# Kernel optimization log

Measured on AMD Instinct MI355X. Metric: run time of the kernel, lower is better.

## Reference

```python
import jax, jax.numpy as jnp
import numpy as np

EPS = 1e-12
N_NODES = 100000
N_EDGES = 1600000
IN_CH = 8
N_CLASSES = 16
MAX_ORDER = 1
N_RINGS = 2


def setup_inputs() -> dict:
    key = jax.random.key(0)
    k0, k1, k2, k3, k4 = jax.random.split(key, 5)
    x = jax.random.normal(k0, (N_NODES, IN_CH), dtype=jnp.float32)
    edge_index = jax.random.randint(k1, (2, N_EDGES), 0, N_NODES)
    precomp = jax.random.normal(k2, (N_EDGES, MAX_ORDER + 1, N_RINGS, 2), dtype=jnp.float32)
    connection = jax.random.normal(k3, (N_EDGES, 2), dtype=jnp.float32)
    # n_orders = (prev_order+1)*(max_order+1) with default prev_order=1 -> 2*(max_order+1)
    n_orders = 2 * (MAX_ORDER + 1)
    radial_profile = jax.random.normal(k4, (n_orders, N_RINGS, N_CLASSES, IN_CH), dtype=jnp.float32) * 0.1
    bias = jnp.zeros((N_CLASSES,), dtype=jnp.float32)
    return dict(x=x, edge_index=edge_index, precomp=precomp,
                connection=connection, radial_profile=radial_profile, bias=bias)


def reference(x, edge_index, precomp, connection, radial_profile, bias):
    # x is stacked with zeros -> complex features with a single stream (M=1, input_order=0).
    # Since input_order==0 only, `connection` (parallel transport) is never applied.
    N = x.shape[0]
    O1 = MAX_ORDER + 1
    src = edge_index[0]  # aggregation targets (flow='target_to_source')
    tgt = edge_index[1]  # gathered neighbours (x_j)
    xjr = x[tgt]                      # [E, F] real part
    xji = jnp.zeros_like(xjr)         # [E, F] imaginary part (zeros by construction)
    # m = |output_order - 0| = output_order; sign = np.sign(m) -> 0 for order 0, +1 otherwise
    signs = jnp.sign(jnp.arange(O1, dtype=x.dtype))
    pre_re = jnp.transpose(precomp[..., 0], (0, 2, 1))          # [E, R, O1]
    pre_im = jnp.transpose(precomp[..., 1], (0, 2, 1)) * signs  # [E, R, O1]
    a_re = xjr[:, None, :, None]      # [E, 1, F, 1]
    a_im = xji[:, None, :, None]
    b_re = pre_re[:, :, None, :]      # [E, R, 1, O1]
    b_im = pre_im[:, :, None, :]
    msg_re = a_re * b_re - a_im * b_im   # [E, R, F, O1]
    msg_im = a_re * b_im + a_im * b_re
    aggr_re = jax.ops.segment_sum(msg_re, src, num_segments=N)  # [N, R, F, O1]
    aggr_im = jax.ops.segment_sum(msg_im, src, num_segments=N)
    # update: m_idx = 0*(max_order+1)+output_order, offset=False
    prof = radial_profile[:O1]        # [O1, R, C, F]
    out_re = jnp.einsum('orcf,nrfo->noc', prof, aggr_re)  # [N, O1, C]
    out_im = jnp.einsum('orcf,nrfo->noc', prof, aggr_im)
    mag = jnp.sqrt(jnp.maximum(out_re * out_re + out_im * out_im, EPS))  # [N, O1, C]
    logits = mag.sum(axis=1) + bias   # [N, C]
    return jax.nn.log_softmax(logits, axis=1)
```

## Files before the change

kernel.cpp:

```cpp
#include <hip/hip_runtime.h>
#include <hip/hip_fp16.h>

#define N_NODES 100000
#define N_EDGES 1600000
#define IN_CH 8
#define N_CLASSES 16

#define NPB 64
#define NPB_SHIFT 6
#define NB ((N_NODES + NPB - 1) / NPB)
#define NB_PAD 1568
#define BIN_T 2048
#define NBLK ((N_EDGES + BIN_T - 1) / BIN_T)
#define MAX_BE 1536

union H2I { __half2 h; int i; };

#define RECBUF_OFF  0
#define BCNT_OFF    ((size_t)N_EDGES * 16)
#define COLSUM_OFF  (BCNT_OFF + (size_t)NBLK * NB_PAD * 4)
#define GBASE_OFF   (COLSUM_OFF + (size_t)NB_PAD * 4)
#define BIN_WS_BYTES (GBASE_OFF + ((size_t)NB + 4) * 4)

#define AGGR_RE_FLOATS (N_NODES * 32)
#define AGGR_IM_FLOATS (N_NODES * 16)
#define WS_FLOATS (AGGR_RE_FLOATS + AGGR_IM_FLOATS)
#define WS_F4 (WS_FLOATS / 4)


__global__ __launch_bounds__(1024) void hist_kernel(const int* __restrict__ ei,
                                                    int* __restrict__ bcnt) {
    __shared__ int h[NB_PAD];
    int t = threadIdx.x;
    for (int i = t; i < NB_PAD; i += 1024) h[i] = 0;
    __syncthreads();
    int base = blockIdx.x * BIN_T;
    int end = base + BIN_T; if (end > N_EDGES) end = N_EDGES;
    for (int e = base + t; e < end; e += 1024)
        atomicAdd(&h[ei[e] >> NPB_SHIFT], 1);
    __syncthreads();
    for (int i = t; i < NB_PAD; i += 1024)
        bcnt[(size_t)blockIdx.x * NB_PAD + i] = h[i];
}

__global__ __launch_bounds__(1024) void colscan_kernel(int* __restrict__ bcnt,
                                                       int* __restrict__ colsum) {
    __shared__ int sbuf[16][65];
    int t = threadIdx.x;
    int r64 = t >> 4, c = t & 15;
    int c0 = blockIdx.x * 16;
    int vals[13];
    int partial = 0;
#pragma unroll
    for (int k = 0; k < 13; ++k) {
        int row = r64 * 13 + k;
        int v = (row < NBLK) ? bcnt[(size_t)row * NB_PAD + c0 + c] : 0;
        vals[k] = v;
        partial += v;
    }
    sbuf[c][r64] = partial;
    __syncthreads();
#pragma unroll
    for (int d = 1; d < 64; d <<= 1) {
        int u = (r64 >= d) ? sbuf[c][r64 - d] : 0;
        __syncthreads();
        sbuf[c][r64] += u;
        __syncthreads();
    }
    int running = sbuf[c][r64] - partial;
#pragma unroll
    for (int k = 0; k < 13; ++k) {
        int row = r64 * 13 + k;
        if (row < NBLK) bcnt[(size_t)row * NB_PAD + c0 + c] = running;
        running += vals[k];
    }
    if (r64 == 63) colsum[c0 + c] = sbuf[c][63];
}

__global__ __launch_bounds__(1024) void base_kernel(const int* __restrict__ colsum,
                                                    int* __restrict__ gbase) {
    __shared__ int buf[1024];
    int t = threadIdx.x;
    int i0 = 2 * t, i1 = 2 * t + 1;
    int v0 = (i0 < NB) ? colsum[i0] : 0;
    int v1 = (i1 < NB) ? colsum[i1] : 0;
    buf[t] = v0 + v1;
    __syncthreads();
#pragma unroll
    for (int d = 1; d < 1024; d <<= 1) {
        int u = (t >= d) ? buf[t - d] : 0;
        __syncthreads();
        buf[t] += u;
        __syncthreads();
    }
    int excl = buf[t] - (v0 + v1);
    if (i0 < NB) gbase[i0] = excl;
    if (i1 < NB) gbase[i1] = excl + v0;
    if (t == 1023) gbase[NB] = buf[1023];
}

__global__ __launch_bounds__(1024) void bin_kernel(
    const int* __restrict__ ei, const float* __restrict__ precomp,
    const int* __restrict__ bcnt, const int* __restrict__ gbase,
    int4* __restrict__ recbuf) {
    __shared__ int lbase[NB];
    __shared__ int lcnt[NB];
    int t = threadIdx.x;
    for (int i = t; i < NB; i += 1024) {
        lbase[i] = gbase[i] + bcnt[(size_t)blockIdx.x * NB_PAD + i];
        lcnt[i] = 0;
    }
    __syncthreads();
    int base = blockIdx.x * BIN_T;
    int end = base + BIN_T; if (end > N_EDGES) end = N_EDGES;
    for (int e = base + t; e < end; e += 1024) {
        int src = ei[e];
        int tgt = ei[N_EDGES + e];
        int b = src >> NPB_SHIFT;
        int rank = atomicAdd(&lcnt[b], 1);
        size_t pos = (size_t)(lbase[b] + rank);
        const float4* pc = (const float4*)(precomp + (size_t)e * 8);
        float4 q0 = pc[0], q1 = pc[1];
        H2I u0, u1, u2;
        u0.h = __floats2half2_rn(q0.x, q0.z);
        u1.h = __floats2half2_rn(q1.x, q1.y);
        u2.h = __floats2half2_rn(q1.z, q1.w);
        int packed = tgt | ((src & (NPB - 1)) << 17);
        recbuf[pos] = make_int4(u0.i, u1.i, u2.i, packed);
    }
}

__global__ __launch_bounds__(512) void aggregate_kernel(
    const int* __restrict__ gbase, const int4* __restrict__ recbuf,
    const float* __restrict__ x,
    const float* __restrict__ prof, const float* __restrict__ bias,
    float* __restrict__ out) {
    __shared__ float sprof[512];
    __shared__ int cnt[NPB];
    __shared__ int start[NPB];
    __shared__ int cur[NPB];
    __shared__ int skey[MAX_BE];
    __shared__ int srec[MAX_BE];
    __shared__ float acc[NPB * 48];

    int t = threadIdx.x, b = blockIdx.x;
    sprof[t] = prof[t];
    if (t < NPB) cnt[t] = 0;
    __syncthreads();

    int lo = gbase[b], hi = gbase[b + 1];
    int n = hi - lo; if (n > MAX_BE) n = MAX_BE;
    const int* ri = (const int*)recbuf;

    for (int k = t; k < n; k += 512) {
        int key = ri[(size_t)(lo + k) * 4 + 3];
        skey[k] = key;
        atomicAdd(&cnt[((unsigned)key) >> 17], 1);
    }
    __syncthreads();

    if (t < 64) {
        int v = cnt[t];
        int s = v;
#pragma unroll
        for (int d = 1; d < 64; d <<= 1) {
            int u = __shfl_up(s, d, 64);
            if (t >= d) s += u;
        }
        start[t] = s - v;
        cur[t] = s - v;
    }
    __syncthreads();

    for (int k = t; k < n; k += 512) {
        int packed = skey[k];
        int nl = ((unsigned)packed) >> 17;
        int p = atomicAdd(&cur[nl], 1);
        srec[p] = (packed & 0x1FFFF) | (k << 17);
    }
    __syncthreads();

    int nl = t >> 3, f = t & 7;
    float a0r0 = 0.f, a1r0 = 0.f, aIr0 = 0.f, a0r1 = 0.f, a1r1 = 0.f, aIr1 = 0.f;
    int s0 = start[nl], n0 = cnt[nl];
    for (int k = 0; k < n0; ++k) {
        int rec = srec[s0 + k];
        int slot = ((unsigned)rec) >> 17;
        int tgt = rec & 0x1FFFF;
        int4 rv = recbuf[(size_t)(lo + slot)];
        H2I u0, u1, u2; u0.i = rv.x; u1.i = rv.y; u2.i = rv.z;
        float2 f0 = __half22float2(u0.h);
        float2 f1 = __half22float2(u1.h);
        float2 f2 = __half22float2(u2.h);
        float xv = x[tgt * IN_CH + f];
        a0r0 = fmaf(xv, f0.x, a0r0);
        a0r1 = fmaf(xv, f0.y, a0r1);
        a1r0 = fmaf(xv, f1.x, a1r0);
        aIr0 = fmaf(xv, f1.y, aIr0);
        a1r1 = fmaf(xv, f2.x, a1r1);
        aIr1 = fmaf(xv, f2.y, aIr1);
    }
    float* a = acc + nl * 48;
    a[f * 3 + 0] = a0r0;  a[f * 3 + 1] = a1r0;  a[f * 3 + 2] = aIr0;
    a[24 + f * 3 + 0] = a0r1;  a[24 + f * 3 + 1] = a1r1;  a[24 + f * 3 + 2] = aIr1;
    __syncthreads();

#pragma unroll
    for (int pass = 0; pass < 2; ++pass) {
        int nl2 = pass * 32 + (t >> 4);
        int c = t & 15;
        int gnode = b * NPB + nl2;
        if (gnode < N_NODES) {
            float re0 = 0.f, re1 = 0.f, im1 = 0.f;
#pragma unroll
            for (int rr = 0; rr < 2; ++rr) {
#pragma unroll
                for (int ff = 0; ff < 8; ++ff) {
                    int idx = nl2 * 48 + rr * 24 + ff * 3;
                    float w0 = sprof[(0 * 2 + rr) * 128 + c * 8 + ff];
                    float w1 = sprof[(1 * 2 + rr) * 128 + c * 8 + ff];
                    re0 = fmaf(w0, acc[idx + 0], re0);
                    re1 = fmaf(w1, acc[idx + 1], re1);
                    im1 = fmaf(w1, acc[idx + 2], im1);
                }
            }
            float mag = sqrtf(fmaxf(re0 * re0, 1e-12f)) +
                        sqrtf(fmaxf(re1 * re1 + im1 * im1, 1e-12f));
            float logit = mag + bias[c];
            float m = logit;
#pragma unroll
            for (int o = 1; o < 16; o <<= 1) m = fmaxf(m, __shfl_xor(m, o, 16));
            float ex = __expf(logit - m);
            float s = ex;
#pragma unroll
            for (int o = 1; o < 16; o <<= 1) s += __shfl_xor(s, o, 16);
            out[gnode * N_CLASSES + c] = (logit - m) - logf(s);
        }
    }
}


__global__ __launch_bounds__(256) void zero_ws_kernel(float4* __restrict__ ws, int n4) {
    int i = blockIdx.x * blockDim.x + threadIdx.x;
    if (i < n4) ws[i] = make_float4(0.f, 0.f, 0.f, 0.f);
}

__global__ __launch_bounds__(256) void edge_kernel(
    const int* __restrict__ ei, const float* __restrict__ x,
    const float* __restrict__ precomp,
    float* __restrict__ aggrRe, float* __restrict__ aggrIm) {
    int gid = blockIdx.x * blockDim.x + threadIdx.x;
    int e = gid >> 3;
    int f = gid & 7;
    if (e >= N_EDGES) return;
    int src = ei[e];
    int tgt = ei[N_EDGES + e];
    float xv = x[tgt * IN_CH + f];
    const float4* pc = (const float4*)(precomp + (size_t)e * 8);
    float4 p0 = pc[0], p1 = pc[1];
    float* ar = aggrRe + (size_t)src * 32;
    atomicAdd(ar + ((0 * 8 + f) * 2 + 0), xv * p0.x);
    atomicAdd(ar + ((1 * 8 + f) * 2 + 0), xv * p0.z);
    atomicAdd(ar + ((0 * 8 + f) * 2 + 1), xv * p1.x);
    atomicAdd(ar + ((1 * 8 + f) * 2 + 1), xv * p1.z);
    float* ai = aggrIm + (size_t)src * 16;
    atomicAdd(ai + (0 * 8 + f), xv * p1.y);
    atomicAdd(ai + (1 * 8 + f), xv * p1.w);
}

__global__ __launch_bounds__(256) void node_kernel(
    const float* __restrict__ aggrRe, const float* __restrict__ aggrIm,
    const float* __restrict__ prof, const float* __restrict__ bias,
    float* __restrict__ out) {
    __shared__ float sprof[512];
    for (int i = threadIdx.x; i < 512; i += blockDim.x) sprof[i] = prof[i];
    __syncthreads();
    int gid = blockIdx.x * blockDim.x + threadIdx.x;
    int n = gid >> 4;
    int c = gid & 15;
    if (n >= N_NODES) return;
    const float* ar = aggrRe + (size_t)n * 32;
    const float* ai = aggrIm + (size_t)n * 16;
    float re0 = 0.f, re1 = 0.f, im1 = 0.f;
#pragma unroll
    for (int r = 0; r < 2; ++r)
#pragma unroll
        for (int f = 0; f < 8; ++f) {
            float a0 = ar[(r * 8 + f) * 2 + 0];
            float a1 = ar[(r * 8 + f) * 2 + 1];
            float aI = ai[r * 8 + f];
            float w0 = sprof[(0 * 2 + r) * 128 + c * 8 + f];
            float w1 = sprof[(1 * 2 + r) * 128 + c * 8 + f];
            re0 = fmaf(w0, a0, re0);
            re1 = fmaf(w1, a1, re1);
            im1 = fmaf(w1, aI, im1);
        }
    float mag = sqrtf(fmaxf(re0 * re0, 1e-12f)) +
                sqrtf(fmaxf(re1 * re1 + im1 * im1, 1e-12f));
    float logit = mag + bias[c];
    float m = logit;
#pragma unroll
    for (int o = 1; o < 16; o <<= 1) m = fmaxf(m, __shfl_xor(m, o, 16));
    float ex = __expf(logit - m);
    float s = ex;
#pragma unroll
    for (int o = 1; o < 16; o <<= 1) s += __shfl_xor(s, o, 16);
    out[n * N_CLASSES + c] = (logit - m) - logf(s);
}


extern "C" void kernel_launch(void* const* d_in, const int* in_sizes, int n_in,
                              void* d_out, int out_size, void* d_ws, size_t ws_size,
                              hipStream_t stream) {
    const float* x       = (const float*)d_in[0];
    const int*   ei      = (const int*)d_in[1];
    const float* precomp = (const float*)d_in[2];
    const float* prof    = (const float*)d_in[4];
    const float* bias    = (const float*)d_in[5];
    float* out = (float*)d_out;

    if (ws_size >= BIN_WS_BYTES) {
        char* ws = (char*)d_ws;
        int4* recbuf = (int4*)(ws + RECBUF_OFF);
        int* bcnt    = (int*)(ws + BCNT_OFF);
        int* colsum  = (int*)(ws + COLSUM_OFF);
        int* gbase   = (int*)(ws + GBASE_OFF);

        hist_kernel<<<NBLK, 1024, 0, stream>>>(ei, bcnt);
        colscan_kernel<<<NB_PAD / 16, 1024, 0, stream>>>(bcnt, colsum);
        base_kernel<<<1, 1024, 0, stream>>>(colsum, gbase);
        bin_kernel<<<NBLK, 1024, 0, stream>>>(ei, precomp, bcnt, gbase, recbuf);
        aggregate_kernel<<<NB, 512, 0, stream>>>(gbase, recbuf, x, prof, bias, out);
    } else {
        float* aggrRe = (float*)d_ws;
        float* aggrIm = aggrRe + AGGR_RE_FLOATS;
        zero_ws_kernel<<<(WS_F4 + 255) / 256, 256, 0, stream>>>((float4*)d_ws, WS_F4);
        int edge_threads = N_EDGES * 8;
        edge_kernel<<<(edge_threads + 255) / 256, 256, 0, stream>>>(ei, x, precomp, aggrRe, aggrIm);
        int node_threads = N_NODES * 16;
        node_kernel<<<(node_threads + 255) / 256, 256, 0, stream>>>(aggrRe, aggrIm, prof, bias, out);
    }
}
```

Measured before the change: 79.44 us.

## Stage binned records in LDS and write them out coalesced by bucket

The bin kernel now does a local histogram and a block-wide scan, sorts each tile's 2000 records into shared memory by destination bucket, and then writes them to global memory in contiguous runs rather than scattering each record on its own. Tiles become exactly 2000 edges with 800 blocks, which removes the bounds checks. Each block's histogram row is placed through a permuted tile_row mapping, which appears intended to change the order in which blocks' ranges are interleaved. The cost is extra shared memory (about 56KB of LDS), an extra pass over the edge indices, and more barriers.

```diff
diff --git a/kernel.cpp b/kernel.cpp
--- a/kernel.cpp
+++ b/kernel.cpp
@@ -10,9 +10,11 @@
 #define NPB_SHIFT 6
 #define NB ((N_NODES + NPB - 1) / NPB)
 #define NB_PAD 1568
-#define BIN_T 2048
-#define NBLK ((N_EDGES + BIN_T - 1) / BIN_T)
+#define BIN_T 2000
+#define NBLK 800
 #define MAX_BE 1536
+
+__device__ __forceinline__ int tile_row(int b) { return ((b & 7) * 100) + (b >> 3); }
 
 union H2I { __half2 h; int i; };
 
@@ -35,12 +37,13 @@
     for (int i = t; i < NB_PAD; i += 1024) h[i] = 0;
     __syncthreads();
     int base = blockIdx.x * BIN_T;
-    int end = base + BIN_T; if (end > N_EDGES) end = N_EDGES;
+    int end = base + BIN_T;
     for (int e = base + t; e < end; e += 1024)
         atomicAdd(&h[ei[e] >> NPB_SHIFT], 1);
     __syncthreads();
+    size_t row = (size_t)tile_row(blockIdx.x);
     for (int i = t; i < NB_PAD; i += 1024)
-        bcnt[(size_t)blockIdx.x * NB_PAD + i] = h[i];
+        bcnt[row * NB_PAD + i] = h[i];
 }
 
 __global__ __launch_bounds__(1024) void colscan_kernel(int* __restrict__ bcnt,
@@ -99,26 +102,64 @@
     if (t == 1023) gbase[NB] = buf[1023];
 }
 
-__global__ __launch_bounds__(1024) void bin_kernel(
+__global__ __launch_bounds__(512) void bin_kernel(
     const int* __restrict__ ei, const float* __restrict__ precomp,
     const int* __restrict__ bcnt, const int* __restrict__ gbase,
     int4* __restrict__ recbuf) {
+    __shared__ int4 srec[BIN_T];
+    __shared__ unsigned short sb[BIN_T];
     __shared__ int lbase[NB];
     __shared__ int lcnt[NB];
+    __shared__ unsigned short tstart[NB];
+    __shared__ int sscan[512];
+
     int t = threadIdx.x;
-    for (int i = t; i < NB; i += 1024) {
-        lbase[i] = gbase[i] + bcnt[(size_t)blockIdx.x * NB_PAD + i];
+    size_t row = (size_t)tile_row(blockIdx.x);
+    for (int i = t; i < NB; i += 512) {
+        lbase[i] = gbase[i] + bcnt[row * NB_PAD + i];
         lcnt[i] = 0;
     }
     __syncthreads();
+
     int base = blockIdx.x * BIN_T;
-    int end = base + BIN_T; if (end > N_EDGES) end = N_EDGES;
-    for (int e = base + t; e < end; e += 1024) {
+
+#pragma unroll
+    for (int k = t; k < BIN_T; k += 512)
+        atomicAdd(&lcnt[ei[base + k] >> NPB_SHIFT], 1);
+    __syncthreads();
+
+    {
+        int i0 = t * 4;
+        int v0 = (i0 + 0 < NB) ? lcnt[i0 + 0] : 0;
+        int v1 = (i0 + 1 < NB) ? lcnt[i0 + 1] : 0;
+        int v2 = (i0 + 2 < NB) ? lcnt[i0 + 2] : 0;
+        int v3 = (i0 + 3 < NB) ? lcnt[i0 + 3] : 0;
+        int tot = v0 + v1 + v2 + v3;
+        sscan[t] = tot;
+        __syncthreads();
+#pragma unroll
+        for (int d = 1; d < 512; d <<= 1) {
+            int u = (t >= d) ? sscan[t - d] : 0;
+            __syncthreads();
+            sscan[t] += u;
+            __syncthreads();
+        }
+        int run = sscan[t] - tot;
+        if (i0 + 0 < NB) { tstart[i0 + 0] = (unsigned short)run; }  run += v0;
+        if (i0 + 1 < NB) { tstart[i0 + 1] = (unsigned short)run; }  run += v1;
+        if (i0 + 2 < NB) { tstart[i0 + 2] = (unsigned short)run; }  run += v2;
+        if (i0 + 3 < NB) { tstart[i0 + 3] = (unsigned short)run; }
+    }
+    __syncthreads();
+    for (int i = t; i < NB; i += 512) lcnt[i] = 0;
+    __syncthreads();
+
+#pragma unroll
+    for (int k = t; k < BIN_T; k += 512) {
+        int e = base + k;
         int src = ei[e];
         int tgt = ei[N_EDGES + e];
         int b = src >> NPB_SHIFT;
-        int rank = atomicAdd(&lcnt[b], 1);
-        size_t pos = (size_t)(lbase[b] + rank);
         const float4* pc = (const float4*)(precomp + (size_t)e * 8);
         float4 q0 = pc[0], q1 = pc[1];
         H2I u0, u1, u2;
@@ -126,7 +167,18 @@
         u1.h = __floats2half2_rn(q1.x, q1.y);
         u2.h = __floats2half2_rn(q1.z, q1.w);
         int packed = tgt | ((src & (NPB - 1)) << 17);
-        recbuf[pos] = make_int4(u0.i, u1.i, u2.i, packed);
+        int rank = atomicAdd(&lcnt[b], 1);
+        int s = (int)tstart[b] + rank;
+        srec[s] = make_int4(u0.i, u1.i, u2.i, packed);
+        sb[s] = (unsigned short)b;
+    }
+    __syncthreads();
+
+#pragma unroll
+    for (int s = t; s < BIN_T; s += 512) {
+        int b = (int)sb[s];
+        int pos = lbase[b] + (s - (int)tstart[b]);
+        recbuf[(size_t)pos] = srec[s];
     }
 }
 
@@ -329,7 +381,7 @@
         hist_kernel<<<NBLK, 1024, 0, stream>>>(ei, bcnt);
         colscan_kernel<<<NB_PAD / 16, 1024, 0, stream>>>(bcnt, colsum);
         base_kernel<<<1, 1024, 0, stream>>>(colsum, gbase);
-        bin_kernel<<<NBLK, 1024, 0, stream>>>(ei, precomp, bcnt, gbase, recbuf);
+        bin_kernel<<<NBLK, 512, 0, stream>>>(ei, precomp, bcnt, gbase, recbuf);
         aggregate_kernel<<<NB, 512, 0, stream>>>(gbase, recbuf, x, prof, bias, out);
     } else {
         float* aggrRe = (float*)d_ws;
```

Measured after the change: 73.44 us. 1.08x faster.
